# Optimization experiments

Hardware: AMD Instinct MI355X
Metric: run time of the kernel (lower is better)

## Reference

```python
import jax, jax.numpy as jnp
import numpy as np

N_POINTS = 200
LEVEL_DIM = 4
NUM_LEVELS = 3
RESOLUTIONS = (8, 16, 32)  # base_resolution=8, per-level scale 2
BATCH = 32768


def _sph_to_cart(theta, phi):
    st = jnp.sin(theta)
    return jnp.stack([st * jnp.cos(phi), st * jnp.sin(phi), jnp.cos(theta)], axis=-1)


def _sample_points(x):
    # x: [B,4] -> points on segment between two unit-sphere points: [B, N_POINTS, 3]
    p1 = _sph_to_cart(x[:, 0], x[:, 1])
    p2 = _sph_to_cart(x[:, 2], x[:, 3])
    t = jnp.linspace(0.0, 1.0, N_POINTS, dtype=x.dtype).reshape(1, N_POINTS, 1)
    return p1[:, None, :] + (p2 - p1)[:, None, :] * t


def _grid_interp(points, table, R):
    # points: [B,S,3] in [-1,1]; table: [(R+1)^3, D] dense grid. Trilinear interp.
    u = jnp.clip((points + 1.0) * 0.5, 0.0, 1.0) * R
    p0 = jnp.clip(jnp.floor(u).astype(jnp.int32), 0, R - 1)
    f = u - p0.astype(u.dtype)
    Rp1 = R + 1
    out = jnp.zeros(points.shape[:-1] + (table.shape[-1],), dtype=table.dtype)
    for c in range(8):  # fixed 8 trilinear corners
        off = np.array([(c >> 2) & 1, (c >> 1) & 1, c & 1], dtype=np.int32)
        idx = p0 + off
        lin = (idx[..., 0] * Rp1 + idx[..., 1]) * Rp1 + idx[..., 2]
        w = jnp.prod(jnp.where(off == 1, f, 1.0 - f), axis=-1)
        out = out + w[..., None] * table[lin]
    return out


def setup_inputs() -> dict:
    key = jax.random.key(0)
    ks = jax.random.split(key, 8)
    pi = 3.14159265
    x = jax.random.uniform(ks[0], (BATCH, 4), dtype=jnp.float32) * pi
    grid0 = jax.random.normal(ks[1], ((RESOLUTIONS[0] + 1) ** 3, LEVEL_DIM), jnp.float32) * 0.1
    grid1 = jax.random.normal(ks[2], ((RESOLUTIONS[1] + 1) ** 3, LEVEL_DIM), jnp.float32) * 0.1
    grid2 = jax.random.normal(ks[3], ((RESOLUTIONS[2] + 1) ** 3, LEVEL_DIM), jnp.float32) * 0.1
    w_label = jax.random.normal(ks[4], (NUM_LEVELS, 1), jnp.float32) * 0.5
    b_label = jnp.zeros((1,), jnp.float32)
    w_rgb = jax.random.normal(ks[5], (NUM_LEVELS * (LEVEL_DIM - 1), 3), jnp.float32) * 0.3
    b_rgb = jnp.zeros((3,), jnp.float32)
    return {"x": x, "grid0": grid0, "grid1": grid1, "grid2": grid2,
            "w_label": w_label, "b_label": b_label, "w_rgb": w_rgb, "b_rgb": b_rgb}


def reference(x, grid0, grid1, grid2, w_label, b_label, w_rgb, b_rgb):
    # torch wraps ray sampling in no_grad -> stop_gradient
    points = jax.lax.stop_gradient(_sample_points(x))  # [B,S,3]
    enc = jnp.concatenate(
        [_grid_interp(points, g, R) for g, R in zip((grid0, grid1, grid2), RESOLUTIONS)],
        axis=-1)  # [B,S,12]
    labels_in = enc[:, :, ::LEVEL_DIM]                      # [B,S,3]
    all_prob = jax.nn.sigmoid(labels_in @ w_label + b_label)  # [B,S,1]
    output_hits = jnp.max(all_prob, axis=1)                 # [B,1]
    mask = np.ones(NUM_LEVELS * LEVEL_DIM, dtype=bool)
    mask[::LEVEL_DIM] = False
    rgb_feats = enc[:, :, mask]                             # [B,S,9]
    hit = (all_prob > 0.5).astype(enc.dtype)
    idx_first = jnp.argmax(hit, axis=1)                     # [B,1] first sample with prob>0.5 (0 if none)
    idx3 = jnp.broadcast_to(idx_first[:, :, None], (rgb_feats.shape[0], 1, rgb_feats.shape[2]))
    gathered = jnp.take_along_axis(rgb_feats, idx3, axis=1)[:, 0, :]  # [B,9]
    output_rgb = jax.nn.sigmoid(gathered @ w_rgb + b_rgb)   # [B,3]
    return (output_hits, output_rgb)
```

## Files before the change

### kernel.cpp

```cpp
#include <hip/hip_runtime.h>
#include <math.h>

#define NPTS 200
#define L33   33
#define NLAT  35937
#define NPREP (NLAT * 4)

template<int R>
__device__ __forceinline__ float tri_label(const float* __restrict__ g,
                                           float ux, float uy, float uz) {
    constexpr int Rp1 = R + 1;
    constexpr int SX  = Rp1 * Rp1;
    int ix = min((int)ux, R - 1);
    int iy = min((int)uy, R - 1);
    int iz = min((int)uz, R - 1);
    float fx = ux - (float)ix, fy = uy - (float)iy, fz = uz - (float)iz;
    int b = (ix * Rp1 + iy) * Rp1 + iz;
    float v000 = g[4*b],            v001 = g[4*(b+1)];
    float v010 = g[4*(b+Rp1)],      v011 = g[4*(b+Rp1+1)];
    float v100 = g[4*(b+SX)],       v101 = g[4*(b+SX+1)];
    float v110 = g[4*(b+SX+Rp1)],   v111 = g[4*(b+SX+Rp1+1)];
    float c00 = fmaf(fz, v001 - v000, v000);
    float c01 = fmaf(fz, v011 - v010, v010);
    float c10 = fmaf(fz, v101 - v100, v100);
    float c11 = fmaf(fz, v111 - v110, v110);
    float c0  = fmaf(fy, c01 - c00, c00);
    float c1  = fmaf(fy, c11 - c10, c10);
    return fmaf(fx, c1 - c0, c0);
}

__global__ __launch_bounds__(256)
void prep_kernel(const float* __restrict__ g0, const float* __restrict__ g1,
                 const float* __restrict__ g2, const float* __restrict__ wl,
                 const float* __restrict__ bl, float* __restrict__ Pf) {
    int id = blockIdx.x * blockDim.x + threadIdx.x;
    if (id >= NPREP) return;
    int c  = id & 3;
    int jj = id >> 2;
    int ix = jj % L33;
    int r  = jj / L33;
    int iz = r % L33;
    int iy = r / L33;
    int jy = min(iy + (c >> 1), L33 - 1);
    int jz = min(iz + (c & 1),  L33 - 1);
    float fx = (float)ix, fy = (float)jy, fz = (float)jz;
    float L0 = tri_label<8 >(g0, fx * 0.25f, fy * 0.25f, fz * 0.25f);
    float L1 = tri_label<16>(g1, fx * 0.5f,  fy * 0.5f,  fz * 0.5f);
    float L2 = g2[4 * ((ix * L33 + jy) * L33 + jz)];
    Pf[id] = bl[0] + wl[0] * L0 + wl[1] * L1 + wl[2] * L2;
}

template<int R>
__device__ __forceinline__ void rgb_corner(const float* __restrict__ g,
                                           float cx, float cy, float cz,
                                           int dx, int dy, int dz,
                                           float* f3) {
    constexpr int Rp1 = R + 1;
    float ux = cx * (float)R, uy = cy * (float)R, uz = cz * (float)R;
    int ix = min((int)ux, R - 1);
    int iy = min((int)uy, R - 1);
    int iz = min((int)uz, R - 1);
    float fx = ux - (float)ix, fy = uy - (float)iy, fz = uz - (float)iz;
    int idx = ((ix + dx) * Rp1 + (iy + dy)) * Rp1 + (iz + dz);
    float w = (dx ? fx : 1.0f - fx) * (dy ? fy : 1.0f - fy) * (dz ? fz : 1.0f - fz);
    float4 v = *reinterpret_cast<const float4*>(g + 4 * idx);
    f3[0] = w * v.y;
    f3[1] = w * v.z;
    f3[2] = w * v.w;
}

__global__ __launch_bounds__(256, 4)
void rays_kernel(const float* __restrict__ x,
                 const float4* __restrict__ P,
                 const float* __restrict__ g0,
                 const float* __restrict__ g1,
                 const float* __restrict__ g2,
                 const float* __restrict__ wr,
                 const float* __restrict__ br,
                 float* __restrict__ out_hits,
                 float* __restrict__ out_rgb,
                 int n)
{
    const int tid = blockIdx.x * blockDim.x + threadIdx.x;
    const int ray = tid >> 3;
    const int sub = (int)(threadIdx.x & 7);
    if (ray >= n) return;

    const float th1 = x[ray * 4 + 0];
    const float ph1 = x[ray * 4 + 1];
    const float th2 = x[ray * 4 + 2];
    const float ph2 = x[ray * 4 + 3];
    float s1 = __sinf(th1), c1 = __cosf(th1);
    float s2 = __sinf(th2), c2 = __cosf(th2);
    float p1x = s1 * __cosf(ph1), p1y = s1 * __sinf(ph1), p1z = c1;
    float p2x = s2 * __cosf(ph2), p2y = s2 * __sinf(ph2), p2z = c2;
    const float dxr = p2x - p1x, dyr = p2y - p1y, dzr = p2z - p1z;

    const float inv = 1.0f / (float)(NPTS - 1);
    const float sc  = 16.0f * inv;

    const float bx = fmaf(p1x, 16.0f, 16.0f);
    const float by = fmaf(p1y, 16.0f, 16.0f);
    const float bz = fmaf(p1z, 16.0f, 16.0f);
    const float dux = dxr * sc, duy = dyr * sc, duz = dzr * sc;

    const float subf = (float)sub;
    float maxlogit = -INFINITY;
    int firsthit = NPTS;

#pragma unroll
    for (int i = 0; i < 25; ++i) {
        float tf = subf + (float)(8 * i);
        float ux = fmaf(tf, dux, bx);
        float uy = fmaf(tf, duy, by);
        float uz = fmaf(tf, duz, bz);
        int ix = min((int)ux, 31);
        int iy = min((int)uy, 31);
        int iz = min((int)uz, 31);
        float fx = ux - (float)ix;
        float fy = uy - (float)iy;
        float fz = uz - (float)iz;
        int jj = (iy * L33 + iz) * L33 + ix;
        const float4* p = P + jj;
        float4 q0 = p[0];
        float4 q1 = p[1];
        float mx = fmaf(fx, q1.x - q0.x, q0.x);
        float my = fmaf(fx, q1.y - q0.y, q0.y);
        float mz = fmaf(fx, q1.z - q0.z, q0.z);
        float mw = fmaf(fx, q1.w - q0.w, q0.w);
        float r0 = fmaf(fz, my - mx, mx);
        float r1 = fmaf(fz, mw - mz, mz);
        float logit = fmaf(fy, r1 - r0, r0);
        maxlogit = fmaxf(maxlogit, logit);
        if (logit > 0.0f) firsthit = min(firsthit, 8 * i + sub);
    }

#pragma unroll
    for (int m = 4; m >= 1; m >>= 1) {
        maxlogit = fmaxf(maxlogit, __shfl_xor(maxlogit, m, 64));
        firsthit = min(firsthit, __shfl_xor(firsthit, m, 64));
    }

    const int tsel = (firsthit >= NPTS) ? 0 : firsthit;
    {
        float tt = (float)tsel * inv;
        float px = fmaf(dxr, tt, p1x);
        float py = fmaf(dyr, tt, p1y);
        float pz = fmaf(dzr, tt, p1z);
        float cx = fminf(fmaxf(fmaf(px, 0.5f, 0.5f), 0.0f), 1.0f);
        float cy = fminf(fmaxf(fmaf(py, 0.5f, 0.5f), 0.0f), 1.0f);
        float cz = fminf(fmaxf(fmaf(pz, 0.5f, 0.5f), 0.0f), 1.0f);
        const int dx = (sub >> 2) & 1, dy = (sub >> 1) & 1, dz = sub & 1;
        float feat[9];
        rgb_corner<8 >(g0, cx, cy, cz, dx, dy, dz, &feat[0]);
        rgb_corner<16>(g1, cx, cy, cz, dx, dy, dz, &feat[3]);
        rgb_corner<32>(g2, cx, cy, cz, dx, dy, dz, &feat[6]);
        float acc[3];
#pragma unroll
        for (int c = 0; c < 3; ++c) {
            float a = 0.0f;
#pragma unroll
            for (int f = 0; f < 9; ++f) a = fmaf(feat[f], wr[f * 3 + c], a);
            acc[c] = a;
        }
#pragma unroll
        for (int m = 4; m >= 1; m >>= 1) {
#pragma unroll
            for (int c = 0; c < 3; ++c)
                acc[c] += __shfl_xor(acc[c], m, 64);
        }
        if (sub == 0) {
            out_hits[ray] = 1.0f / (1.0f + __expf(-maxlogit));
#pragma unroll
            for (int c = 0; c < 3; ++c)
                out_rgb[ray * 3 + c] = 1.0f / (1.0f + __expf(-(acc[c] + br[c])));
        }
    }
}

extern "C" void kernel_launch(void* const* d_in, const int* in_sizes, int n_in,
                              void* d_out, int out_size, void* d_ws, size_t ws_size,
                              hipStream_t stream) {
    const float* x  = (const float*)d_in[0];
    const float* g0 = (const float*)d_in[1];
    const float* g1 = (const float*)d_in[2];
    const float* g2 = (const float*)d_in[3];
    const float* wl = (const float*)d_in[4];
    const float* bl = (const float*)d_in[5];
    const float* wr = (const float*)d_in[6];
    const float* br = (const float*)d_in[7];

    const int n = in_sizes[0] / 4;
    float* out_hits = (float*)d_out;
    float* out_rgb  = (float*)d_out + n;

    float* Pf = (float*)d_ws;

    prep_kernel<<<(NPREP + 255) / 256, 256, 0, stream>>>(g0, g1, g2, wl, bl, Pf);

    const int block = 256;
    const int grid = (n * 8 + block - 1) / block;
    rays_kernel<<<grid, block, 0, stream>>>(x, (const float4*)Pf, g0, g1, g2,
                                            wr, br, out_hits, out_rgb, n);
}
```

Measured before the change: 21.35 us.

## Use fp16 per-cell corner table with fp32 fallback for ambiguous hit tests

Splits prep into a lattice-label pass and a pass that builds per-cell 8-corner tables in both fp16 (16 B per cell) and fp32. The ray loop reads one 16-byte fp16 record per sample instead of two float4 loads, halving gather traffic. Samples whose logit lies within a relative error bound of zero are re-checked with the fp32 table so the first-hit index stays exact. maxlogit is now computed from fp16 data, which adds small error to the hit probability, and the extra prep launch and fallback loop add overhead.

```diff
diff --git a/kernel.cpp b/kernel.cpp
--- a/kernel.cpp
+++ b/kernel.cpp
@@ -1,10 +1,15 @@
 #include <hip/hip_runtime.h>
+#include <hip/hip_fp16.h>
 #include <math.h>
 
 #define NPTS 200
 #define L33   33
 #define NLAT  35937
-#define NPREP (NLAT * 4)
+#define NCELL 32768
+#define NPREP (NCELL * 8)
+
+#define WS_C32_OFF   (NCELL * 16)
+#define WS_TLAT_OFF  (WS_C32_OFF + NCELL * 32)
 
 template<int R>
 __device__ __forceinline__ float tri_label(const float* __restrict__ g,
@@ -30,24 +35,38 @@
 }
 
 __global__ __launch_bounds__(256)
-void prep_kernel(const float* __restrict__ g0, const float* __restrict__ g1,
-                 const float* __restrict__ g2, const float* __restrict__ wl,
-                 const float* __restrict__ bl, float* __restrict__ Pf) {
+void prep1_kernel(const float* __restrict__ g0, const float* __restrict__ g1,
+                  const float* __restrict__ g2, const float* __restrict__ wl,
+                  const float* __restrict__ bl, float* __restrict__ T) {
+    int i = blockIdx.x * blockDim.x + threadIdx.x;
+    if (i >= NLAT) return;
+    int jz = i % L33;
+    int r  = i / L33;
+    int jy = r % L33;
+    int jx = r / L33;
+    float fx = (float)jx, fy = (float)jy, fz = (float)jz;
+    float L0 = tri_label<8 >(g0, fx * 0.25f, fy * 0.25f, fz * 0.25f);
+    float L1 = tri_label<16>(g1, fx * 0.5f,  fy * 0.5f,  fz * 0.5f);
+    float L2 = g2[4 * i];
+    T[i] = bl[0] + wl[0] * L0 + wl[1] * L1 + wl[2] * L2;
+}
+
+__global__ __launch_bounds__(256)
+void prep2_kernel(const float* __restrict__ T, __half* __restrict__ H,
+                  float* __restrict__ C) {
     int id = blockIdx.x * blockDim.x + threadIdx.x;
     if (id >= NPREP) return;
-    int c  = id & 3;
-    int jj = id >> 2;
-    int ix = jj % L33;
-    int r  = jj / L33;
-    int iz = r % L33;
-    int iy = r / L33;
-    int jy = min(iy + (c >> 1), L33 - 1);
-    int jz = min(iz + (c & 1),  L33 - 1);
-    float fx = (float)ix, fy = (float)jy, fz = (float)jz;
-    float L0 = tri_label<8 >(g0, fx * 0.25f, fy * 0.25f, fz * 0.25f);
-    float L1 = tri_label<16>(g1, fx * 0.5f,  fy * 0.5f,  fz * 0.5f);
-    float L2 = g2[4 * ((ix * L33 + jy) * L33 + jz)];
-    Pf[id] = bl[0] + wl[0] * L0 + wl[1] * L1 + wl[2] * L2;
+    int c    = id & 7;
+    int cell = id >> 3;
+    int ix = cell & 31;
+    int iz = (cell >> 5) & 31;
+    int iy = cell >> 10;
+    int jx = ix + ((c >> 2) & 1);
+    int jy = iy + ((c >> 1) & 1);
+    int jz = iz + (c & 1);
+    float v = T[(jx * L33 + jy) * L33 + jz];
+    C[id] = v;
+    H[id] = __float2half(v);
 }
 
 template<int R>
@@ -71,7 +90,8 @@
 
 __global__ __launch_bounds__(256, 4)
 void rays_kernel(const float* __restrict__ x,
-                 const float4* __restrict__ P,
+                 const __half* __restrict__ H,
+                 const float4* __restrict__ C,
                  const float* __restrict__ g0,
                  const float* __restrict__ g1,
                  const float* __restrict__ g2,
@@ -106,7 +126,8 @@
 
     const float subf = (float)sub;
     float maxlogit = -INFINITY;
-    int firsthit = NPTS;
+    int fc = NPTS;
+    unsigned smask = 0u;
 
 #pragma unroll
     for (int i = 0; i < 25; ++i) {
@@ -120,28 +141,73 @@
         float fx = ux - (float)ix;
         float fy = uy - (float)iy;
         float fz = uz - (float)iz;
-        int jj = (iy * L33 + iz) * L33 + ix;
-        const float4* p = P + jj;
+        int idx = (iy << 10) | (iz << 5) | ix;
+        uint4 raw = *reinterpret_cast<const uint4*>(
+                        reinterpret_cast<const unsigned char*>(H) + ((size_t)idx << 4));
+        float2 a00 = __half22float2(*reinterpret_cast<const __half2*>(&raw.x));
+        float2 a01 = __half22float2(*reinterpret_cast<const __half2*>(&raw.y));
+        float2 a10 = __half22float2(*reinterpret_cast<const __half2*>(&raw.z));
+        float2 a11 = __half22float2(*reinterpret_cast<const __half2*>(&raw.w));
+        float b00 = fmaf(fx, a10.x - a00.x, a00.x);
+        float b01 = fmaf(fx, a10.y - a00.y, a00.y);
+        float b10 = fmaf(fx, a11.x - a01.x, a01.x);
+        float b11 = fmaf(fx, a11.y - a01.y, a01.y);
+        float r0 = fmaf(fz, b01 - b00, b00);
+        float r1 = fmaf(fz, b11 - b10, b10);
+        float logit = fmaf(fy, r1 - r0, r0);
+        float ma = fmaxf(fmaxf(fmaxf(fabsf(a00.x), fabsf(a00.y)),
+                               fmaxf(fabsf(a01.x), fabsf(a01.y))),
+                         fmaxf(fmaxf(fabsf(a10.x), fabsf(a10.y)),
+                               fmaxf(fabsf(a11.x), fabsf(a11.y))));
+        float thr = 1.5e-3f * ma;
+        maxlogit = fmaxf(maxlogit, logit);
+        int tcur = 8 * i + sub;
+        fc = (logit > thr) ? min(fc, tcur) : fc;
+        smask |= (fabsf(logit) <= thr) ? (1u << i) : 0u;
+    }
+
+#pragma unroll
+    for (int m = 4; m >= 1; m >>= 1) {
+        maxlogit = fmaxf(maxlogit, __shfl_xor(maxlogit, m, 64));
+        fc = min(fc, __shfl_xor(fc, m, 64));
+    }
+
+    int fh = fc;
+    unsigned mm = smask;
+    while (mm) {
+        int i = __builtin_ctz(mm);
+        mm &= mm - 1;
+        int t = 8 * i + sub;
+        if (t >= fh) break;
+        float tf = (float)t;
+        float ux = fmaf(tf, dux, bx);
+        float uy = fmaf(tf, duy, by);
+        float uz = fmaf(tf, duz, bz);
+        int ix = min((int)ux, 31);
+        int iy = min((int)uy, 31);
+        int iz = min((int)uz, 31);
+        float fx = ux - (float)ix;
+        float fy = uy - (float)iy;
+        float fz = uz - (float)iz;
+        int idx = (iy << 10) | (iz << 5) | ix;
+        const float4* p = C + 2 * idx;
         float4 q0 = p[0];
         float4 q1 = p[1];
-        float mx = fmaf(fx, q1.x - q0.x, q0.x);
-        float my = fmaf(fx, q1.y - q0.y, q0.y);
-        float mz = fmaf(fx, q1.z - q0.z, q0.z);
-        float mw = fmaf(fx, q1.w - q0.w, q0.w);
-        float r0 = fmaf(fz, my - mx, mx);
-        float r1 = fmaf(fz, mw - mz, mz);
-        float logit = fmaf(fy, r1 - r0, r0);
-        maxlogit = fmaxf(maxlogit, logit);
-        if (logit > 0.0f) firsthit = min(firsthit, 8 * i + sub);
-    }
-
-#pragma unroll
-    for (int m = 4; m >= 1; m >>= 1) {
-        maxlogit = fmaxf(maxlogit, __shfl_xor(maxlogit, m, 64));
-        firsthit = min(firsthit, __shfl_xor(firsthit, m, 64));
-    }
-
-    const int tsel = (firsthit >= NPTS) ? 0 : firsthit;
+        float mx_ = fmaf(fx, q1.x - q0.x, q0.x);
+        float my_ = fmaf(fx, q1.y - q0.y, q0.y);
+        float mz_ = fmaf(fx, q1.z - q0.z, q0.z);
+        float mw_ = fmaf(fx, q1.w - q0.w, q0.w);
+        float r0_ = fmaf(fz, my_ - mx_, mx_);
+        float r1_ = fmaf(fz, mw_ - mz_, mz_);
+        float lg  = fmaf(fy, r1_ - r0_, r0_);
+        if (lg > 0.0f) { fh = t; break; }
+    }
+
+#pragma unroll
+    for (int m = 4; m >= 1; m >>= 1)
+        fh = min(fh, __shfl_xor(fh, m, 64));
+
+    const int tsel = (fh >= NPTS) ? 0 : fh;
     {
         float tt = (float)tsel * inv;
         float px = fmaf(dxr, tt, p1x);
@@ -194,12 +260,16 @@
     float* out_hits = (float*)d_out;
     float* out_rgb  = (float*)d_out + n;
 
-    float* Pf = (float*)d_ws;
-
-    prep_kernel<<<(NPREP + 255) / 256, 256, 0, stream>>>(g0, g1, g2, wl, bl, Pf);
+    __half* H   = (__half*)d_ws;
+    float*  C32 = (float*)((char*)d_ws + WS_C32_OFF);
+    float*  T   = (float*)((char*)d_ws + WS_TLAT_OFF);
+
+    prep1_kernel<<<(NLAT  + 255) / 256, 256, 0, stream>>>(g0, g1, g2, wl, bl, T);
+    prep2_kernel<<<(NPREP + 255) / 256, 256, 0, stream>>>(T, H, C32);
 
     const int block = 256;
     const int grid = (n * 8 + block - 1) / block;
-    rays_kernel<<<grid, block, 0, stream>>>(x, (const float4*)Pf, g0, g1, g2,
-                                            wr, br, out_hits, out_rgb, n);
-}
+    rays_kernel<<<grid, block, 0, stream>>>(x, H, (const float4*)C32,
+                                            g0, g1, g2, wr, br,
+                                            out_hits, out_rgb, n);
+}
```

Result: slower. 38.00 us (+78.0%).

## Stage scalar label lattice in LDS and track first hit with bitmask

Applied to the files above, without the earlier changes.

Prep now writes one scalar label logit per lattice point instead of a four-wide corner-packed table. Each 1024-thread rays block copies the whole 33^3 lattice (about 144KB) into shared memory, then does the eight trilinear corner reads from LDS rather than two float4 global gathers per sample. Per-thread first-hit tracking becomes a 25-bit mask resolved with count-trailing-zeros. The trade-offs are a serialized per-block staging phase, one large block per CU, possible LDS bank conflicts on the gathers, and the removal of the ray-count bound check, which assumes n is a multiple of 128.

```diff
diff --git a/kernel.cpp b/kernel.cpp
--- a/kernel.cpp
+++ b/kernel.cpp
@@ -3,8 +3,8 @@
 
 #define NPTS 200
 #define L33   33
+#define L33SQ 1089
 #define NLAT  35937
-#define NPREP (NLAT * 4)
 
 template<int R>
 __device__ __forceinline__ float tri_label(const float* __restrict__ g,
@@ -29,25 +29,21 @@
     return fmaf(fx, c1 - c0, c0);
 }
 
-__global__ __launch_bounds__(256)
-void prep_kernel(const float* __restrict__ g0, const float* __restrict__ g1,
-                 const float* __restrict__ g2, const float* __restrict__ wl,
-                 const float* __restrict__ bl, float* __restrict__ Pf) {
-    int id = blockIdx.x * blockDim.x + threadIdx.x;
-    if (id >= NPREP) return;
-    int c  = id & 3;
-    int jj = id >> 2;
-    int ix = jj % L33;
-    int r  = jj / L33;
-    int iz = r % L33;
-    int iy = r / L33;
-    int jy = min(iy + (c >> 1), L33 - 1);
-    int jz = min(iz + (c & 1),  L33 - 1);
-    float fx = (float)ix, fy = (float)jy, fz = (float)jz;
+__global__ __launch_bounds__(128)
+void prep1_kernel(const float* __restrict__ g0, const float* __restrict__ g1,
+                  const float* __restrict__ g2, const float* __restrict__ wl,
+                  const float* __restrict__ bl, float* __restrict__ T) {
+    int i = blockIdx.x * blockDim.x + threadIdx.x;
+    if (i >= NLAT) return;
+    int jz = i % L33;
+    int r  = i / L33;
+    int jy = r % L33;
+    int jx = r / L33;
+    float fx = (float)jx, fy = (float)jy, fz = (float)jz;
     float L0 = tri_label<8 >(g0, fx * 0.25f, fy * 0.25f, fz * 0.25f);
     float L1 = tri_label<16>(g1, fx * 0.5f,  fy * 0.5f,  fz * 0.5f);
-    float L2 = g2[4 * ((ix * L33 + jy) * L33 + jz)];
-    Pf[id] = bl[0] + wl[0] * L0 + wl[1] * L1 + wl[2] * L2;
+    float L2 = g2[4 * i];
+    T[i] = bl[0] + wl[0] * L0 + wl[1] * L1 + wl[2] * L2;
 }
 
 template<int R>
@@ -69,22 +65,25 @@
     f3[2] = w * v.w;
 }
 
-__global__ __launch_bounds__(256, 4)
+__global__ __launch_bounds__(1024, 4)
 void rays_kernel(const float* __restrict__ x,
-                 const float4* __restrict__ P,
+                 const float* __restrict__ T,
                  const float* __restrict__ g0,
                  const float* __restrict__ g1,
                  const float* __restrict__ g2,
                  const float* __restrict__ wr,
                  const float* __restrict__ br,
                  float* __restrict__ out_hits,
-                 float* __restrict__ out_rgb,
-                 int n)
+                 float* __restrict__ out_rgb)
 {
-    const int tid = blockIdx.x * blockDim.x + threadIdx.x;
-    const int ray = tid >> 3;
-    const int sub = (int)(threadIdx.x & 7);
-    if (ray >= n) return;
+    extern __shared__ float Tl[];
+    const int tid = (int)threadIdx.x;
+
+    for (int i = tid; i < NLAT; i += 1024) Tl[i] = T[i];
+    __syncthreads();
+
+    const int ray = (int)blockIdx.x * 128 + (tid >> 3);
+    const int sub = tid & 7;
 
     const float th1 = x[ray * 4 + 0];
     const float ph1 = x[ray * 4 + 1];
@@ -106,7 +105,7 @@
 
     const float subf = (float)sub;
     float maxlogit = -INFINITY;
-    int firsthit = NPTS;
+    unsigned hmask = 0u;
 
 #pragma unroll
     for (int i = 0; i < 25; ++i) {
@@ -120,28 +119,31 @@
         float fx = ux - (float)ix;
         float fy = uy - (float)iy;
         float fz = uz - (float)iz;
-        int jj = (iy * L33 + iz) * L33 + ix;
-        const float4* p = P + jj;
-        float4 q0 = p[0];
-        float4 q1 = p[1];
-        float mx = fmaf(fx, q1.x - q0.x, q0.x);
-        float my = fmaf(fx, q1.y - q0.y, q0.y);
-        float mz = fmaf(fx, q1.z - q0.z, q0.z);
-        float mw = fmaf(fx, q1.w - q0.w, q0.w);
-        float r0 = fmaf(fz, my - mx, mx);
-        float r1 = fmaf(fz, mw - mz, mz);
-        float logit = fmaf(fy, r1 - r0, r0);
+        int b = (ix * L33 + iy) * L33 + iz;
+        float v000 = Tl[b],               v001 = Tl[b + 1];
+        float v010 = Tl[b + L33],         v011 = Tl[b + L33 + 1];
+        float v100 = Tl[b + L33SQ],       v101 = Tl[b + L33SQ + 1];
+        float v110 = Tl[b + L33SQ + L33], v111 = Tl[b + L33SQ + L33 + 1];
+        float a00 = fmaf(fz, v001 - v000, v000);
+        float a01 = fmaf(fz, v011 - v010, v010);
+        float a10 = fmaf(fz, v101 - v100, v100);
+        float a11 = fmaf(fz, v111 - v110, v110);
+        float b0  = fmaf(fy, a01 - a00, a00);
+        float b1  = fmaf(fy, a11 - a10, a10);
+        float logit = fmaf(fx, b1 - b0, b0);
         maxlogit = fmaxf(maxlogit, logit);
-        if (logit > 0.0f) firsthit = min(firsthit, 8 * i + sub);
+        hmask |= (logit > 0.0f) ? (1u << i) : 0u;
     }
+
+    int fc = hmask ? (8 * __builtin_ctz(hmask) + sub) : NPTS;
 
 #pragma unroll
     for (int m = 4; m >= 1; m >>= 1) {
         maxlogit = fmaxf(maxlogit, __shfl_xor(maxlogit, m, 64));
-        firsthit = min(firsthit, __shfl_xor(firsthit, m, 64));
+        fc = min(fc, __shfl_xor(fc, m, 64));
     }
 
-    const int tsel = (firsthit >= NPTS) ? 0 : firsthit;
+    const int tsel = (fc >= NPTS) ? 0 : fc;
     {
         float tt = (float)tsel * inv;
         float px = fmaf(dxr, tt, p1x);
@@ -194,12 +196,11 @@
     float* out_hits = (float*)d_out;
     float* out_rgb  = (float*)d_out + n;
 
-    float* Pf = (float*)d_ws;
-
-    prep_kernel<<<(NPREP + 255) / 256, 256, 0, stream>>>(g0, g1, g2, wl, bl, Pf);
-
-    const int block = 256;
-    const int grid = (n * 8 + block - 1) / block;
-    rays_kernel<<<grid, block, 0, stream>>>(x, (const float4*)Pf, g0, g1, g2,
-                                            wr, br, out_hits, out_rgb, n);
-}
+    float* T = (float*)d_ws;
+
+    prep1_kernel<<<(NLAT + 127) / 128, 128, 0, stream>>>(g0, g1, g2, wl, bl, T);
+
+    const int grid = n / 128;
+    rays_kernel<<<grid, 1024, NLAT * sizeof(float), stream>>>(
+        x, T, g0, g1, g2, wr, br, out_hits, out_rgb);
+}
```

Measured after the change: 21.89 us. 2.5% more time.
